# Optimization experiments

Measured on AMD Instinct MI355X. Metric: run time of the kernel, lower is better.

The kernel has to match this reference:

```python
import jax, jax.numpy as jnp
import numpy as np

EPS = 1e-5


def _layernorm(x, w, b):
    mu = jnp.mean(x, axis=-1, keepdims=True)
    var = jnp.var(x, axis=-1, keepdims=True)
    return (x - mu) * jax.lax.rsqrt(var + EPS) * w + b


def setup_inputs() -> dict:
    key = jax.random.key(0)
    ks = jax.random.split(key, 5)
    B, I, H = 8192, 1024, 1024
    inp = {
        "input": jax.random.normal(ks[0], (B, I), dtype=jnp.float32),
        "hx": jax.random.normal(ks[1], (B, H), dtype=jnp.float32),
        "cx": jax.random.normal(ks[2], (B, H), dtype=jnp.float32),
        # parameters (torch initializes weights with randn; LN weight=1, bias=0)
        "weight_ih": jax.random.normal(ks[3], (4 * H, I), dtype=jnp.float32),
        "weight_hh": jax.random.normal(ks[4], (4 * H, H), dtype=jnp.float32),
        "ln_i_w": jnp.ones((4 * H,), jnp.float32),
        "ln_i_b": jnp.zeros((4 * H,), jnp.float32),
        "ln_h_w": jnp.ones((4 * H,), jnp.float32),
        "ln_h_b": jnp.zeros((4 * H,), jnp.float32),
        "ln_c_w": jnp.ones((H,), jnp.float32),
        "ln_c_b": jnp.zeros((H,), jnp.float32),
    }
    return inp


def reference(input, hx, cx, weight_ih, weight_hh,
              ln_i_w, ln_i_b, ln_h_w, ln_h_b, ln_c_w, ln_c_b):
    # gate pre-activations: [B, 4H]
    igates = _layernorm(input @ weight_ih.T, ln_i_w, ln_i_b)
    hgates = _layernorm(hx @ weight_hh.T, ln_h_w, ln_h_b)
    gates = igates + hgates
    ingate, forgetgate, cellgate, outgate = jnp.split(gates, 4, axis=-1)
    ingate = jax.nn.sigmoid(ingate)
    forgetgate = jax.nn.sigmoid(forgetgate)
    cellgate = jnp.tanh(cellgate)
    outgate = jax.nn.sigmoid(outgate)
    cy = _layernorm(forgetgate * cx + ingate * cellgate, ln_c_w, ln_c_b)
    hy = outgate * jnp.tanh(cy)  # activation=Tanh, dropout p=0 is identity
    return (hy, cy)
```

## Files before the change

### kernel.cpp

```cpp
#include <hip/hip_runtime.h>
#include <hip/hip_bf16.h>
#include <cstdint>
#include <cstddef>

typedef __bf16 bf16_t;
typedef bf16_t bf16x8 __attribute__((ext_vector_type(8)));
typedef float floatx4 __attribute__((ext_vector_type(4)));

static constexpr int B_ = 8192;
static constexpr int H_ = 1024;
static constexpr int G4 = 4096;
static constexpr int K_ = 1024;

__device__ inline void async16(const void* g, void* l) {
  auto l3 = (__attribute__((address_space(3))) void*)(uint32_t)(uintptr_t)l;
  __builtin_amdgcn_global_load_lds(
      (__attribute__((address_space(1))) void*)(uintptr_t)g, l3, 16, 0, 0);
}

__global__ __launch_bounds__(256) void prep_all(
    const float* __restrict__ input, const float* __restrict__ hx,
    const float* __restrict__ wih, const float* __restrict__ whh,
    bf16_t* __restrict__ Abf, bf16_t* __restrict__ Hbf,
    bf16_t* __restrict__ Wib, bf16_t* __restrict__ Whb) {
  const int bid = blockIdx.x;
  if (bid < 4096) {
    const int nt = B_ * K_ / 16;
    int gid = bid * 256 + threadIdx.x;
    const float* src; bf16_t* dst; int idx;
    if (gid < nt) { src = input; dst = Abf; idx = gid; }
    else          { src = hx;    dst = Hbf; idx = gid - nt; }
    const float4* s4 = (const float4*)src + (size_t)idx * 4;
    const float4 v0 = s4[0], v1 = s4[1], v2 = s4[2], v3 = s4[3];
    bf16x8 o0, o1;
    o0[0] = (bf16_t)v0.x; o0[1] = (bf16_t)v0.y; o0[2] = (bf16_t)v0.z; o0[3] = (bf16_t)v0.w;
    o0[4] = (bf16_t)v1.x; o0[5] = (bf16_t)v1.y; o0[6] = (bf16_t)v1.z; o0[7] = (bf16_t)v1.w;
    o1[0] = (bf16_t)v2.x; o1[1] = (bf16_t)v2.y; o1[2] = (bf16_t)v2.z; o1[3] = (bf16_t)v2.w;
    o1[4] = (bf16_t)v3.x; o1[5] = (bf16_t)v3.y; o1[6] = (bf16_t)v3.z; o1[7] = (bf16_t)v3.w;
    ((bf16x8*)dst)[(size_t)idx * 2]     = o0;
    ((bf16x8*)dst)[(size_t)idx * 2 + 1] = o1;
  } else {
    const int r  = bid - 4096;
    const int rr = r * 2 + (threadIdx.x >> 7);
    const int rp = rr & 4095;
    const float* src = (rr < 4096) ? wih : whh;
    bf16_t*      dst = (rr < 4096) ? Wib : Whb;
    const int h = rp >> 2, g = rp & 3;
    const int rin = g * 1024 + h;
    const int c = (threadIdx.x & 127) * 8;
    const float4 v0 = *(const float4*)(src + (size_t)rin * K_ + c);
    const float4 v1 = *(const float4*)(src + (size_t)rin * K_ + c + 4);
    bf16x8 o;
    o[0] = (bf16_t)v0.x; o[1] = (bf16_t)v0.y; o[2] = (bf16_t)v0.z; o[3] = (bf16_t)v0.w;
    o[4] = (bf16_t)v1.x; o[5] = (bf16_t)v1.y; o[6] = (bf16_t)v1.z; o[7] = (bf16_t)v1.w;
    *(bf16x8*)(dst + (size_t)rp * K_ + c) = o;
  }
}


#define FENCE() asm volatile("" ::: "memory")
#define BARRIER() do { FENCE(); __builtin_amdgcn_s_barrier(); FENCE(); } while (0)

__global__ __launch_bounds__(512, 2) void gemm_bt_dual8(
    const bf16_t* __restrict__ A0, const bf16_t* __restrict__ A1,
    const bf16_t* __restrict__ W0, const bf16_t* __restrict__ W1,
    bf16_t* __restrict__ C0, bf16_t* __restrict__ C1) {
  constexpr int N = G4, K = K_, NT = K_ / 64;

  __shared__ bf16_t ldsA[2][16384];
  __shared__ bf16_t ldsB[2][16384];

  const int flatb = blockIdx.x + (blockIdx.y << 4) + (blockIdx.z << 9);
  const int swzb  = (flatb & 7) * 128 + (flatb >> 3);
  const int bz = swzb >> 9;
  const int by = (swzb >> 4) & 31;
  const int bx = swzb & 15;

  const bf16_t* A = bz ? A1 : A0;
  const bf16_t* W = bz ? W1 : W0;
  bf16_t*       C = bz ? C1 : C0;

  const int tid  = threadIdx.x;
  const int lane = tid & 63;
  const int w    = tid >> 6;
  const int wm   = w >> 2, wn = w & 3;
  const int lrow = lane & 15, quad = lane >> 4;
  const int e    = lrow & 7;

  const int m0 = by * 256;
  const int n0 = bx * 256;

  const int srow   = tid >> 3;
  const int schunk = (tid & 7) ^ (srow & 7);
  const bf16_t* gA = A + (size_t)(m0 + srow) * K + schunk * 8;
  const bf16_t* gB = W + (size_t)(n0 + srow) * K + schunk * 8;
  const int wslot = w * 512;

  const int aBase = (wm * 128 + lrow) * 64 + (quad ^ e) * 8;
  const int bBase = (wn * 64 + lrow) * 64 + (quad ^ e) * 8;

  floatx4 acc[8][4] = {};
  bf16x8 aF[4][2];
  bf16x8 bF[2][2][2];

#define STG_A(p, half, kt) do {                                          \
    bf16_t* _l = &ldsA[p][(half) * 8192 + wslot];                        \
    async16(gA + (size_t)((half) * 128) * K + (kt) * 64, _l);            \
    async16(gA + (size_t)((half) * 128 + 64) * K + (kt) * 64, _l + 4096); \
  } while (0)
#define STG_B(p, half, kt) do {                                          \
    bf16_t* _l = &ldsB[p][(half) * 8192 + wslot];                        \
    async16(gB + (size_t)((half) * 128) * K + (kt) * 64, _l);            \
    async16(gB + (size_t)((half) * 128 + 64) * K + (kt) * 64, _l + 4096); \
  } while (0)

#define LD_A(p, qm) do { _Pragma("unroll")                               \
    for (int i2 = 0; i2 < 4; ++i2) {                                     \
      const int o = aBase + (qm) * 4096 + i2 * 1024;                     \
      aF[i2][0] = *(const bf16x8*)&ldsA[p][o];                           \
      aF[i2][1] = *(const bf16x8*)&ldsA[p][o ^ 32];                      \
    } } while (0)
#define LD_B(p, qn) do { _Pragma("unroll")                               \
    for (int j2 = 0; j2 < 2; ++j2) {                                     \
      const int o = bBase + (qn) * 2048 + j2 * 1024;                     \
      bF[qn][j2][0] = *(const bf16x8*)&ldsB[p][o];                       \
      bF[qn][j2][1] = *(const bf16x8*)&ldsB[p][o ^ 32];                  \
    } } while (0)
#define MFMA_Q(qm, qn) do { _Pragma("unroll")                            \
    for (int i2 = 0; i2 < 4; ++i2) { _Pragma("unroll")                   \
      for (int j2 = 0; j2 < 2; ++j2) {                                   \
        floatx4& c = acc[(qm) * 4 + i2][(qn) * 2 + j2];                  \
        c = __builtin_amdgcn_mfma_f32_16x16x32_bf16(aF[i2][0], bF[qn][j2][0], c, 0, 0, 0); \
        c = __builtin_amdgcn_mfma_f32_16x16x32_bf16(aF[i2][1], bF[qn][j2][1], c, 0, 0, 0); \
      } } } while (0)

  STG_B(0, 0, 0); STG_B(0, 1, 0);
  STG_A(0, 0, 0); STG_A(0, 1, 0);
  STG_B(1, 0, 1); STG_B(1, 1, 1);
  asm volatile("s_waitcnt vmcnt(4)" ::: "memory");
  BARRIER();

#pragma unroll 2
  for (int t = 0; t < NT; ++t) {
    const int p = t & 1, q = p ^ 1;
    const int t1 = (t + 1) & (NT - 1), t2 = (t + 2) & (NT - 1);

    LD_A(p, 0); LD_B(p, 0);
    STG_A(q, 0, t1);
    BARRIER();
    asm volatile("s_waitcnt lgkmcnt(0)" ::: "memory");
    __builtin_amdgcn_sched_barrier(0);
    __builtin_amdgcn_s_setprio(1); MFMA_Q(0, 0); __builtin_amdgcn_s_setprio(0);
    BARRIER();

    LD_B(p, 1);
    STG_A(q, 1, t1);
    BARRIER();
    asm volatile("s_waitcnt lgkmcnt(0)" ::: "memory");
    __builtin_amdgcn_sched_barrier(0);
    __builtin_amdgcn_s_setprio(1); MFMA_Q(0, 1); __builtin_amdgcn_s_setprio(0);
    BARRIER();

    LD_A(p, 1);
    STG_B(p, 0, t2);
    BARRIER();
    asm volatile("s_waitcnt lgkmcnt(0)" ::: "memory");
    __builtin_amdgcn_sched_barrier(0);
    __builtin_amdgcn_s_setprio(1); MFMA_Q(1, 0); __builtin_amdgcn_s_setprio(0);
    BARRIER();

    STG_B(p, 1, t2);
    BARRIER();
    __builtin_amdgcn_s_setprio(1); MFMA_Q(1, 1); __builtin_amdgcn_s_setprio(0);
    asm volatile("s_waitcnt vmcnt(4)" ::: "memory");
    BARRIER();
  }

#pragma unroll
  for (int i = 0; i < 8; ++i) {
    const int mbase = m0 + wm * 128 + i * 16 + quad * 4;
#pragma unroll
    for (int j = 0; j < 4; ++j) {
      const int n = n0 + wn * 64 + j * 16 + lrow;
#pragma unroll
      for (int r = 0; r < 4; ++r)
        C[(size_t)(mbase + r) * N + n] = (bf16_t)acc[i][j][r];
    }
  }
#undef STG_A
#undef STG_B
#undef LD_A
#undef LD_B
#undef MFMA_Q
}

__device__ inline float sigmoid_f(float x) { return 1.0f / (1.0f + __expf(-x)); }
__device__ inline float tanh_f(float x) {
  float e = __expf(2.0f * x);
  return 1.0f - 2.0f / (e + 1.0f);
}

__global__ __launch_bounds__(512) void ln_lstm_epi_lds(
    const bf16_t* __restrict__ IG, const bf16_t* __restrict__ HG,
    const float* __restrict__ cx,
    const float* __restrict__ wi, const float* __restrict__ bi,
    const float* __restrict__ wh, const float* __restrict__ bh,
    const float* __restrict__ wc, const float* __restrict__ bc,
    float* __restrict__ hy_out, float* __restrict__ cy_out) {
  __shared__ float lds[18432];

  const int tid = threadIdx.x;
  const int l = tid & 63;
  const int w = tid >> 6;
  const int b = blockIdx.x * 8 + w;

  const bf16_t* igp = IG + (size_t)b * 4096;
  const bf16_t* hgp = HG + (size_t)b * 4096;

  bf16x8 igv[4][2], hgv[4][2];
  float4 cx4[4];
#pragma unroll
  for (int c = 0; c < 4; ++c) {
    const int n0 = c * 1024 + l * 16;
    igv[c][0] = *(const bf16x8*)(igp + n0);
    igv[c][1] = *(const bf16x8*)(igp + n0 + 8);
    hgv[c][0] = *(const bf16x8*)(hgp + n0);
    hgv[c][1] = *(const bf16x8*)(hgp + n0 + 8);
    cx4[c] = *(const float4*)(cx + (size_t)b * 1024 + c * 256 + l * 4);
  }

#define STAGEP(src, off) do {                                             \
    async16((const float4*)(src) + w * 64 + l,       (float4*)lds + (off) + w * 64); \
    async16((const float4*)(src) + 512 + w * 64 + l, (float4*)lds + (off) + 512 + w * 64); \
  } while (0)
  STAGEP(wi, 0);
  STAGEP(bi, 1024);
  STAGEP(wh, 2048);
  STAGEP(bh, 3072);
  if (w < 4) async16((const float4*)wc + w * 64 + l,
                     (float4*)lds + 4096 + w * 64);
  else       async16((const float4*)bc + (w - 4) * 64 + l,
                     (float4*)lds + 4352 + (w - 4) * 64);
#undef STAGEP
  __syncthreads();

  float si = 0, qi = 0, sh = 0, qh = 0;
#pragma unroll
  for (int c = 0; c < 4; ++c)
#pragma unroll
    for (int hf = 0; hf < 2; ++hf)
#pragma unroll
      for (int e = 0; e < 8; ++e) {
        const float a = (float)igv[c][hf][e], d = (float)hgv[c][hf][e];
        si += a; qi = fmaf(a, a, qi);
        sh += d; qh = fmaf(d, d, qh);
      }
#pragma unroll
  for (int off = 1; off < 64; off <<= 1) {
    si += __shfl_xor(si, off); qi += __shfl_xor(qi, off);
    sh += __shfl_xor(sh, off); qh += __shfl_xor(qh, off);
  }
  const float invN = 1.0f / 4096.0f;
  const float mui = si * invN, muh = sh * invN;
  const float rsi = rsqrtf(fmaxf(qi * invN - mui * mui, 0.0f) + 1e-5f);
  const float rsh = rsqrtf(fmaxf(qh * invN - muh * muh, 0.0f) + 1e-5f);

  float cv[16], ov[16];
  float sc = 0, qc = 0;
#pragma unroll
  for (int c = 0; c < 4; ++c) {
    const int h0 = c * 256 + l * 4;
    float4 wiv[4], biv[4], whv[4], bhv[4];
#pragma unroll
    for (int g = 0; g < 4; ++g) {
      wiv[g] = *(const float4*)&lds[g * 1024 + h0];
      biv[g] = *(const float4*)&lds[4096 + g * 1024 + h0];
      whv[g] = *(const float4*)&lds[8192 + g * 1024 + h0];
      bhv[g] = *(const float4*)&lds[12288 + g * 1024 + h0];
    }
#pragma unroll
    for (int k = 0; k < 4; ++k) {
      float G[4];
#pragma unroll
      for (int g = 0; g < 4; ++g) {
        const int idx = k * 4 + g;
        const float gi = (float)igv[c][idx >> 3][idx & 7];
        const float gh = (float)hgv[c][idx >> 3][idx & 7];
        G[g] = (gi - mui) * rsi * ((const float*)&wiv[g])[k] + ((const float*)&biv[g])[k] +
               (gh - muh) * rsh * ((const float*)&whv[g])[k] + ((const float*)&bhv[g])[k];
      }
      const float in_g = sigmoid_f(G[0]);
      const float fo_g = sigmoid_f(G[1]);
      const float ce_g = tanh_f(G[2]);
      ov[c * 4 + k] = sigmoid_f(G[3]);
      const float cc = fo_g * ((const float*)&cx4[c])[k] + in_g * ce_g;
      cv[c * 4 + k] = cc;
      sc += cc; qc = fmaf(cc, cc, qc);
    }
  }
#pragma unroll
  for (int off = 1; off < 64; off <<= 1) {
    sc += __shfl_xor(sc, off); qc += __shfl_xor(qc, off);
  }
  const float invH = 1.0f / 1024.0f;
  const float muc = sc * invH;
  const float rsc = rsqrtf(fmaxf(qc * invH - muc * muc, 0.0f) + 1e-5f);

#pragma unroll
  for (int c = 0; c < 4; ++c) {
    const int h0 = c * 256 + l * 4;
    const float4 wc4 = *(const float4*)&lds[16384 + h0];
    const float4 bc4 = *(const float4*)&lds[17408 + h0];
    float4 cyv, hyv;
#pragma unroll
    for (int k = 0; k < 4; ++k) {
      const float cyn = (cv[c * 4 + k] - muc) * rsc * ((const float*)&wc4)[k] +
                        ((const float*)&bc4)[k];
      ((float*)&cyv)[k] = cyn;
      ((float*)&hyv)[k] = ov[c * 4 + k] * tanh_f(cyn);
    }
    *(float4*)(cy_out + (size_t)b * 1024 + h0) = cyv;
    *(float4*)(hy_out + (size_t)b * 1024 + h0) = hyv;
  }
}

extern "C" void kernel_launch(void* const* d_in, const int* in_sizes, int n_in,
                              void* d_out, int out_size, void* d_ws, size_t ws_size,
                              hipStream_t stream) {
  const float* input  = (const float*)d_in[0];
  const float* hx     = (const float*)d_in[1];
  const float* cx     = (const float*)d_in[2];
  const float* w_ih   = (const float*)d_in[3];
  const float* w_hh   = (const float*)d_in[4];
  const float* ln_i_w = (const float*)d_in[5];
  const float* ln_i_b = (const float*)d_in[6];
  const float* ln_h_w = (const float*)d_in[7];
  const float* ln_h_b = (const float*)d_in[8];
  const float* ln_c_w = (const float*)d_in[9];
  const float* ln_c_b = (const float*)d_in[10];

  float* out = (float*)d_out;
  float* hy = out;
  float* cy = out + (size_t)B_ * H_;

  bf16_t* Abf = (bf16_t*)d_ws;
  bf16_t* Hbf = Abf + (size_t)B_ * K_;
  bf16_t* Wib = Hbf + (size_t)B_ * K_;
  bf16_t* Whb = Wib + (size_t)G4 * K_;
  bf16_t* IG  = Whb + (size_t)G4 * K_;
  bf16_t* HG  = IG + (size_t)B_ * G4;

  prep_all<<<8192, 256, 0, stream>>>(input, hx, w_ih, w_hh, Abf, Hbf, Wib, Whb);

  gemm_bt_dual8<<<dim3(16, 32, 2), 512, 0, stream>>>(Abf, Hbf, Wib, Whb, IG, HG);

  ln_lstm_epi_lds<<<1024, 512, 0, stream>>>(IG, HG, cx, ln_i_w, ln_i_b,
                                            ln_h_w, ln_h_b, ln_c_w, ln_c_b, hy, cy);
}
```

Measured before the change: 373.4 us.

## Process four rows per wavefront in LSTM epilogue, drop LDS param staging

The epilogue kernel now assigns four batch rows to each wavefront, 16 rows per 256-thread block. LayerNorm weights are read straight from global memory and reused across the four rows instead of being staged in LDS with a barrier. Gate inputs are read twice (once for statistics, once for the activation) instead of held in registers, and the output gate is kept as bf16 to save registers. This amortises parameter loads and removes the barrier, at the cost of extra IG/HG traffic, higher register pressure, bf16 rounding of the output gate, and only 512 blocks in the grid.

```diff
diff --git a/kernel.cpp b/kernel.cpp
--- a/kernel.cpp
+++ b/kernel.cpp
@@ -57,7 +57,6 @@
   }
 }
 
-
 #define FENCE() asm volatile("" ::: "memory")
 #define BARRIER() do { FENCE(); __builtin_amdgcn_s_barrier(); FENCE(); } while (0)
 
@@ -200,127 +199,136 @@
   return 1.0f - 2.0f / (e + 1.0f);
 }
 
-__global__ __launch_bounds__(512) void ln_lstm_epi_lds(
+__global__ __launch_bounds__(256) void ln_lstm_epi4(
     const bf16_t* __restrict__ IG, const bf16_t* __restrict__ HG,
     const float* __restrict__ cx,
     const float* __restrict__ wi, const float* __restrict__ bi,
     const float* __restrict__ wh, const float* __restrict__ bh,
     const float* __restrict__ wc, const float* __restrict__ bc,
     float* __restrict__ hy_out, float* __restrict__ cy_out) {
-  __shared__ float lds[18432];
-
-  const int tid = threadIdx.x;
-  const int l = tid & 63;
-  const int w = tid >> 6;
-  const int b = blockIdx.x * 8 + w;
-
-  const bf16_t* igp = IG + (size_t)b * 4096;
-  const bf16_t* hgp = HG + (size_t)b * 4096;
-
-  bf16x8 igv[4][2], hgv[4][2];
-  float4 cx4[4];
-#pragma unroll
-  for (int c = 0; c < 4; ++c) {
-    const int n0 = c * 1024 + l * 16;
-    igv[c][0] = *(const bf16x8*)(igp + n0);
-    igv[c][1] = *(const bf16x8*)(igp + n0 + 8);
-    hgv[c][0] = *(const bf16x8*)(hgp + n0);
-    hgv[c][1] = *(const bf16x8*)(hgp + n0 + 8);
-    cx4[c] = *(const float4*)(cx + (size_t)b * 1024 + c * 256 + l * 4);
-  }
-
-#define STAGEP(src, off) do {                                             \
-    async16((const float4*)(src) + w * 64 + l,       (float4*)lds + (off) + w * 64); \
-    async16((const float4*)(src) + 512 + w * 64 + l, (float4*)lds + (off) + 512 + w * 64); \
-  } while (0)
-  STAGEP(wi, 0);
-  STAGEP(bi, 1024);
-  STAGEP(wh, 2048);
-  STAGEP(bh, 3072);
-  if (w < 4) async16((const float4*)wc + w * 64 + l,
-                     (float4*)lds + 4096 + w * 64);
-  else       async16((const float4*)bc + (w - 4) * 64 + l,
-                     (float4*)lds + 4352 + (w - 4) * 64);
-#undef STAGEP
-  __syncthreads();
-
-  float si = 0, qi = 0, sh = 0, qh = 0;
-#pragma unroll
-  for (int c = 0; c < 4; ++c)
-#pragma unroll
-    for (int hf = 0; hf < 2; ++hf)
+  const int l  = threadIdx.x & 63;
+  const int wv = threadIdx.x >> 6;
+  const int b0 = blockIdx.x * 16 + wv * 4;
+
+  float si[4] = {}, qi[4] = {}, sh[4] = {}, qh[4] = {};
+#pragma unroll
+  for (int r = 0; r < 4; ++r) {
+    const bf16_t* igp = IG + (size_t)(b0 + r) * 4096;
+    const bf16_t* hgp = HG + (size_t)(b0 + r) * 4096;
+#pragma unroll
+    for (int c = 0; c < 4; ++c) {
+      const int n0 = c * 1024 + l * 16;
+      const bf16x8 a0 = *(const bf16x8*)(igp + n0);
+      const bf16x8 a1 = *(const bf16x8*)(igp + n0 + 8);
+      const bf16x8 d0 = *(const bf16x8*)(hgp + n0);
+      const bf16x8 d1 = *(const bf16x8*)(hgp + n0 + 8);
 #pragma unroll
       for (int e = 0; e < 8; ++e) {
-        const float a = (float)igv[c][hf][e], d = (float)hgv[c][hf][e];
-        si += a; qi = fmaf(a, a, qi);
-        sh += d; qh = fmaf(d, d, qh);
+        const float x0 = (float)a0[e], x1 = (float)a1[e];
+        const float y0 = (float)d0[e], y1 = (float)d1[e];
+        si[r] += x0 + x1; qi[r] = fmaf(x0, x0, fmaf(x1, x1, qi[r]));
+        sh[r] += y0 + y1; qh[r] = fmaf(y0, y0, fmaf(y1, y1, qh[r]));
       }
-#pragma unroll
-  for (int off = 1; off < 64; off <<= 1) {
-    si += __shfl_xor(si, off); qi += __shfl_xor(qi, off);
-    sh += __shfl_xor(sh, off); qh += __shfl_xor(qh, off);
-  }
+    }
+  }
+#pragma unroll
+  for (int off = 1; off < 64; off <<= 1)
+#pragma unroll
+    for (int r = 0; r < 4; ++r) {
+      si[r] += __shfl_xor(si[r], off); qi[r] += __shfl_xor(qi[r], off);
+      sh[r] += __shfl_xor(sh[r], off); qh[r] += __shfl_xor(qh[r], off);
+    }
   const float invN = 1.0f / 4096.0f;
-  const float mui = si * invN, muh = sh * invN;
-  const float rsi = rsqrtf(fmaxf(qi * invN - mui * mui, 0.0f) + 1e-5f);
-  const float rsh = rsqrtf(fmaxf(qh * invN - muh * muh, 0.0f) + 1e-5f);
-
-  float cv[16], ov[16];
-  float sc = 0, qc = 0;
+  float mui[4], rsi[4], muh[4], rsh[4];
+#pragma unroll
+  for (int r = 0; r < 4; ++r) {
+    mui[r] = si[r] * invN; muh[r] = sh[r] * invN;
+    rsi[r] = rsqrtf(fmaxf(qi[r] * invN - mui[r] * mui[r], 0.0f) + 1e-5f);
+    rsh[r] = rsqrtf(fmaxf(qh[r] * invN - muh[r] * muh[r], 0.0f) + 1e-5f);
+  }
+
+  float  cvv[4][16];
+  bf16x8 ovv[4][2];
+  float  scc[4] = {}, qcc[4] = {};
 #pragma unroll
   for (int c = 0; c < 4; ++c) {
     const int h0 = c * 256 + l * 4;
     float4 wiv[4], biv[4], whv[4], bhv[4];
 #pragma unroll
     for (int g = 0; g < 4; ++g) {
-      wiv[g] = *(const float4*)&lds[g * 1024 + h0];
-      biv[g] = *(const float4*)&lds[4096 + g * 1024 + h0];
-      whv[g] = *(const float4*)&lds[8192 + g * 1024 + h0];
-      bhv[g] = *(const float4*)&lds[12288 + g * 1024 + h0];
-    }
-#pragma unroll
-    for (int k = 0; k < 4; ++k) {
-      float G[4];
-#pragma unroll
-      for (int g = 0; g < 4; ++g) {
-        const int idx = k * 4 + g;
-        const float gi = (float)igv[c][idx >> 3][idx & 7];
-        const float gh = (float)hgv[c][idx >> 3][idx & 7];
-        G[g] = (gi - mui) * rsi * ((const float*)&wiv[g])[k] + ((const float*)&biv[g])[k] +
-               (gh - muh) * rsh * ((const float*)&whv[g])[k] + ((const float*)&bhv[g])[k];
+      wiv[g] = *(const float4*)(wi + g * 1024 + h0);
+      biv[g] = *(const float4*)(bi + g * 1024 + h0);
+      whv[g] = *(const float4*)(wh + g * 1024 + h0);
+      bhv[g] = *(const float4*)(bh + g * 1024 + h0);
+    }
+#pragma unroll
+    for (int r = 0; r < 4; ++r) {
+      const bf16_t* igp = IG + (size_t)(b0 + r) * 4096;
+      const bf16_t* hgp = HG + (size_t)(b0 + r) * 4096;
+      const int n0 = c * 1024 + l * 16;
+      const bf16x8 a0 = *(const bf16x8*)(igp + n0);
+      const bf16x8 a1 = *(const bf16x8*)(igp + n0 + 8);
+      const bf16x8 d0 = *(const bf16x8*)(hgp + n0);
+      const bf16x8 d1 = *(const bf16x8*)(hgp + n0 + 8);
+      const float4 c4 = *(const float4*)(cx + (size_t)(b0 + r) * 1024 + h0);
+#pragma unroll
+      for (int kk = 0; kk < 4; ++kk) {
+        float G[4];
+#pragma unroll
+        for (int g = 0; g < 4; ++g) {
+          const int idx = kk * 4 + g;
+          const float gi = (idx < 8) ? (float)a0[idx] : (float)a1[idx - 8];
+          const float gh = (idx < 8) ? (float)d0[idx] : (float)d1[idx - 8];
+          G[g] = (gi - mui[r]) * rsi[r] * ((const float*)&wiv[g])[kk] +
+                 ((const float*)&biv[g])[kk] +
+                 (gh - muh[r]) * rsh[r] * ((const float*)&whv[g])[kk] +
+                 ((const float*)&bhv[g])[kk];
+        }
+        const float in_g = sigmoid_f(G[0]);
+        const float fo_g = sigmoid_f(G[1]);
+        const float ce_g = tanh_f(G[2]);
+        const float o_g  = sigmoid_f(G[3]);
+        const float cc = fo_g * ((const float*)&c4)[kk] + in_g * ce_g;
+        const int idx = c * 4 + kk;
+        cvv[r][idx] = cc;
+        ovv[r][idx >> 3][idx & 7] = (bf16_t)o_g;
+        scc[r] += cc; qcc[r] = fmaf(cc, cc, qcc[r]);
       }
-      const float in_g = sigmoid_f(G[0]);
-      const float fo_g = sigmoid_f(G[1]);
-      const float ce_g = tanh_f(G[2]);
-      ov[c * 4 + k] = sigmoid_f(G[3]);
-      const float cc = fo_g * ((const float*)&cx4[c])[k] + in_g * ce_g;
-      cv[c * 4 + k] = cc;
-      sc += cc; qc = fmaf(cc, cc, qc);
-    }
-  }
-#pragma unroll
-  for (int off = 1; off < 64; off <<= 1) {
-    sc += __shfl_xor(sc, off); qc += __shfl_xor(qc, off);
-  }
+    }
+  }
+#pragma unroll
+  for (int off = 1; off < 64; off <<= 1)
+#pragma unroll
+    for (int r = 0; r < 4; ++r) {
+      scc[r] += __shfl_xor(scc[r], off); qcc[r] += __shfl_xor(qcc[r], off);
+    }
   const float invH = 1.0f / 1024.0f;
-  const float muc = sc * invH;
-  const float rsc = rsqrtf(fmaxf(qc * invH - muc * muc, 0.0f) + 1e-5f);
+  float muc[4], rsc[4];
+#pragma unroll
+  for (int r = 0; r < 4; ++r) {
+    muc[r] = scc[r] * invH;
+    rsc[r] = rsqrtf(fmaxf(qcc[r] * invH - muc[r] * muc[r], 0.0f) + 1e-5f);
+  }
 
 #pragma unroll
   for (int c = 0; c < 4; ++c) {
     const int h0 = c * 256 + l * 4;
-    const float4 wc4 = *(const float4*)&lds[16384 + h0];
-    const float4 bc4 = *(const float4*)&lds[17408 + h0];
-    float4 cyv, hyv;
-#pragma unroll
-    for (int k = 0; k < 4; ++k) {
-      const float cyn = (cv[c * 4 + k] - muc) * rsc * ((const float*)&wc4)[k] +
-                        ((const float*)&bc4)[k];
-      ((float*)&cyv)[k] = cyn;
-      ((float*)&hyv)[k] = ov[c * 4 + k] * tanh_f(cyn);
-    }
-    *(float4*)(cy_out + (size_t)b * 1024 + h0) = cyv;
-    *(float4*)(hy_out + (size_t)b * 1024 + h0) = hyv;
+    const float4 wc4 = *(const float4*)(wc + h0);
+    const float4 bc4 = *(const float4*)(bc + h0);
+#pragma unroll
+    for (int r = 0; r < 4; ++r) {
+      float4 cyv, hyv;
+#pragma unroll
+      for (int kk = 0; kk < 4; ++kk) {
+        const int idx = c * 4 + kk;
+        const float cyn = (cvv[r][idx] - muc[r]) * rsc[r] *
+                          ((const float*)&wc4)[kk] + ((const float*)&bc4)[kk];
+        ((float*)&cyv)[kk] = cyn;
+        ((float*)&hyv)[kk] = (float)ovv[r][idx >> 3][idx & 7] * tanh_f(cyn);
+      }
+      *(float4*)(cy_out + (size_t)(b0 + r) * 1024 + h0) = cyv;
+      *(float4*)(hy_out + (size_t)(b0 + r) * 1024 + h0) = hyv;
+    }
   }
 }
 
@@ -354,6 +362,6 @@
 
   gemm_bt_dual8<<<dim3(16, 32, 2), 512, 0, stream>>>(Abf, Hbf, Wib, Whb, IG, HG);
 
-  ln_lstm_epi_lds<<<1024, 512, 0, stream>>>(IG, HG, cx, ln_i_w, ln_i_b,
-                                            ln_h_w, ln_h_b, ln_c_w, ln_c_b, hy, cy);
-}
+  ln_lstm_epi4<<<512, 256, 0, stream>>>(IG, HG, cx, ln_i_w, ln_i_b,
+                                        ln_h_w, ln_h_b, ln_c_w, ln_c_b, hy, cy);
+}
```

Measured after the change: 448.9 us. 1.2x slower.
